# Kernel tuning notes

Measured on AMD Instinct MI355X. Metric: run time of the kernel, lower is better.

The kernel has to match this reference:

```python
import jax, jax.numpy as jnp
import numpy as np

CUTOFF = 10.0
K = 32            # max_num_neighbors
NUM_GRAPHS = 64
ATOMS = 128
N = NUM_GRAPHS * ATOMS
HID = 128
FIL = 128
NG = 50           # num_gaussians
LAYERS = 6
MAX_Z = 100
PI = 3.14159265   # constant used verbatim in the torch source


def silu(x):
    return x * jax.nn.sigmoid(x)


def build_graph(pos, batch):
    """Dense cdist + per-node top-K neighbor selection (radius_graph_pure).
    Returns idx[i,k] = k-th nearest neighbor j of center i, and a validity mask.
    Torch edge (row, col) = (j, i): node j receives a message computed from x[i].
    """
    p = jax.lax.stop_gradient(pos)
    d2 = jnp.sum((p[:, None, :] - p[None, :, :]) ** 2, -1)          # [N,N]
    same = batch[:, None] == batch[None, :]
    eye = jnp.eye(p.shape[0], dtype=bool)
    valid = same & (d2 < CUTOFF * CUTOFF) & (~eye)
    dm = jnp.where(valid, d2, jnp.inf)
    neg, idx = jax.lax.top_k(-dm, K)                                 # [N,K]
    return idx, jnp.isfinite(neg)                                    # edge valid iff within mask


def setup_inputs() -> dict:
    key = jax.random.key(0)
    ks = jax.random.split(key, 20)
    s = 0.05
    inp = {
        "pos": jax.random.normal(ks[0], (N, 3), jnp.float32),
        "z": jax.random.randint(ks[1], (N,), 0, MAX_Z),
        "batch": jnp.repeat(jnp.arange(NUM_GRAPHS), ATOMS),
        # parameters (weights stored as [in, out])
        "emb": jax.random.normal(ks[2], (MAX_Z, HID), jnp.float32) * s,
        "mw1": jax.random.normal(ks[3], (LAYERS, NG, FIL), jnp.float32) * s,
        "mb1": jax.random.normal(ks[4], (LAYERS, FIL), jnp.float32) * s,
        "mw2": jax.random.normal(ks[5], (LAYERS, FIL, FIL), jnp.float32) * s,
        "mb2": jax.random.normal(ks[6], (LAYERS, FIL), jnp.float32) * s,
        "l1w": jax.random.normal(ks[7], (LAYERS, HID, FIL), jnp.float32) * s,
        "l1b": jax.random.normal(ks[8], (LAYERS, FIL), jnp.float32) * s,
        "l2w": jax.random.normal(ks[9], (LAYERS, FIL, HID), jnp.float32) * s,
        "l2b": jax.random.normal(ks[10], (LAYERS, HID), jnp.float32) * s,
        "ow1": jax.random.normal(ks[11], (HID, HID // 2), jnp.float32) * s,
        "ob1": jax.random.normal(ks[12], (HID // 2,), jnp.float32) * s,
        "ow2": jax.random.normal(ks[13], (HID // 2, 1), jnp.float32) * s,
        "ob2": jax.random.normal(ks[14], (1,), jnp.float32) * s,
    }
    return inp


def reference(pos, z, batch, emb, mw1, mb1, mw2, mb2, l1w, l1b, l2w, l2b, ow1, ob1, ow2, ob2):
    idx, evalid = build_graph(pos, batch)                 # [N,K], [N,K]
    ev = evalid.astype(pos.dtype)
    diff = pos[idx] - pos[:, None, :]                     # [N,K,3]
    d2e = jnp.sum(diff * diff, -1)
    dist = jnp.sqrt(jnp.where(evalid, d2e, 1.0))          # safe sqrt for masked edges
    offset = jnp.linspace(0.0, CUTOFF, NG)
    width = CUTOFF / (NG - 1)
    rbf = jnp.exp(-0.5 * ((dist[..., None] - offset) / width) ** 2)   # [N,K,NG]
    cval = 0.5 * (jnp.cos(dist * PI / CUTOFF) + 1.0)
    cval = cval * (dist < CUTOFF).astype(pos.dtype) * ev  # zero out invalid edges

    h = emb[z]                                            # [N,HID]
    flat_idx = idx.reshape(-1)                            # receivers (torch row)
    for l in range(LAYERS):
        W = silu(rbf @ mw1[l] + mb1[l]) @ mw2[l] + mb2[l]           # filter MLP
        W = W * cval[..., None]                                       # [N,K,FIL]
        xj = (h @ l1w[l] + l1b[l])[:, None, :]                        # sender = center i
        msg = (xj * W).reshape(N * K, FIL)
        agg = jax.ops.segment_sum(msg, flat_idx, num_segments=N)     # scatter_add at row
        h = h + silu(agg @ l2w[l] + l2b[l])

    out = (silu(h @ ow1 + ob1) @ ow2 + ob2)[:, 0]         # [N]
    return jax.ops.segment_sum(out, batch, num_segments=NUM_GRAPHS)  # [G]
```

## Files before the change

kernel.cpp:

```cpp
#include <hip/hip_runtime.h>
#include <math.h>

typedef unsigned short u16;
typedef unsigned int   u32;
typedef unsigned long long u64;

#define NATOMS 8192
#define GRAPHS 64
#define KNN    32
#define NGAUSS 50
#define HID    128
#define LAYERS 6
#define NTAB   4096
#define SA     136
#define SW1    72
#define SH     132

typedef __attribute__((ext_vector_type(8))) short bf16x8;
typedef __attribute__((ext_vector_type(4))) float f32x4;

__device__ __forceinline__ float bf2f(u16 v) {
    return __uint_as_float(((u32)v) << 16);
}
__device__ __forceinline__ u16 f2bf(float f) {
    u32 u = __float_as_uint(f);
    u32 lsb = (u >> 16) & 1u;
    u += 0x7fffu + lsb;
    return (u16)(u >> 16);
}
__device__ __forceinline__ u32 pkbf(float lo, float hi) {
#if __has_builtin(__builtin_amdgcn_cvt_pk_bf16_f32)
    auto r = __builtin_amdgcn_cvt_pk_bf16_f32(lo, hi);
    u32 u; __builtin_memcpy(&u, &r, 4); return u;
#else
    return (u32)f2bf(lo) | ((u32)f2bf(hi) << 16);
#endif
}
__device__ __forceinline__ float silu_f(float x) {
    return x * __builtin_amdgcn_rcpf(1.0f + __expf(-x));
}
__device__ __forceinline__ bf16x8 ldfrag(const u16* p) {
    return *(const bf16x8*)__builtin_assume_aligned(p, 16);
}
__device__ __forceinline__ u64 shfl_xor_u64(u64 v, int mask) {
    u32 lo = (u32)v, hi = (u32)(v >> 32);
    lo = (u32)__shfl_xor((int)lo, mask, 64);
    hi = (u32)__shfl_xor((int)hi, mask, 64);
    return ((u64)hi << 32) | lo;
}
__device__ __forceinline__ float ldf(const void* p, int i, bool f32in) {
    return f32in ? ((const float*)p)[i] : bf2f(((const u16*)p)[i]);
}
union U8 { bf16x8 v; u32 w[4]; };

__global__ void probe_kernel(const u16* __restrict__ raw, int* __restrict__ flag,
                             int* __restrict__ rev_cnt, float* __restrict__ gsum,
                             int* __restrict__ done_cnt, int* __restrict__ xflags) {
    __shared__ int s;
    int t = threadIdx.x;
    if (t == 0) s = 0;
    __syncthreads();
    float x = bf2f(raw[2 * t]);
    if (!(fabsf(x) < 1000.0f)) atomicOr(&s, 1);
    for (int i = t; i < NATOMS; i += 256) rev_cnt[i] = 0;
    for (int i = t; i < 2048; i += 256) xflags[i] = 0;
    if (t < GRAPHS) gsum[t] = 0.0f;
    if (t == 0) *done_cnt = 0;
    __syncthreads();
    if (t == 0) *flag = s;
}

#define NARR 9
struct IngestDesc {
    const void* src[NARR];
    void*       dst[NARR];
    int         n[NARR];
};

#define NB_BUILD 2048
#define NB_PREP  768

__launch_bounds__(256)
__global__ void setup_kernel(const void* __restrict__ pos,
                             const void* __restrict__ l1w, const void* __restrict__ l2w,
                             u16* __restrict__ l1wt, u16* __restrict__ l2wt,
                             IngestDesc d, int total_ing,
                             const int* __restrict__ flag,
                             int* __restrict__ rev_cnt, u32* __restrict__ rev) {
    int bid = blockIdx.x;
    bool f32in = (*flag != 0);
    if (bid < NB_BUILD) {
        int wv = threadIdx.x >> 6, lane = threadIdx.x & 63;
        int t = bid * 4 + wv;
        int tl = t & 127;
        int base = t & ~127;
        float cx = ldf(pos, t * 3 + 0, f32in);
        float cy = ldf(pos, t * 3 + 1, f32in);
        float cz = ldf(pos, t * 3 + 2, f32in);
        u64 key[2];
#pragma unroll
        for (int c = 0; c < 2; ++c) {
            int j = lane + c * 64;
            float jx = ldf(pos, (base + j) * 3 + 0, f32in);
            float jy = ldf(pos, (base + j) * 3 + 1, f32in);
            float jz = ldf(pos, (base + j) * 3 + 2, f32in);
            float dx = __fsub_rn(cx, jx);
            float dy = __fsub_rn(cy, jy);
            float dz = __fsub_rn(cz, jz);
            float d2 = __fadd_rn(__fadd_rn(__fmul_rn(dx, dx), __fmul_rn(dy, dy)),
                                 __fmul_rn(dz, dz));
            bool valid = (j != tl) && (d2 < 100.0f);
            key[c] = valid ? ((((u64)__float_as_uint(d2)) << 32) | (u32)j) : ~0ULL;
        }
#pragma unroll
        for (int k = 2; k <= 128; k <<= 1) {
#pragma unroll
            for (int j = k >> 1; j > 0; j >>= 1) {
                if (j == 64) {
                    u64 lo = key[0] < key[1] ? key[0] : key[1];
                    u64 hi = key[0] < key[1] ? key[1] : key[0];
                    key[0] = lo; key[1] = hi;
                } else {
#pragma unroll
                    for (int r = 0; r < 2; ++r) {
                        u64 o = shfl_xor_u64(key[r], j);
                        u32 ii = (u32)(r * 64 + lane);
                        bool dir = ((ii & (u32)k) == 0);
                        bool lower = ((ii & (u32)j) == 0);
                        bool keep_min = (dir == lower);
                        bool less = key[r] < o;
                        key[r] = (less == keep_min) ? key[r] : o;
                    }
                }
            }
        }
        if (lane < KNN) {
            u64 m = key[0];
            if (m != ~0ULL) {
                float d2 = __uint_as_float((u32)(m >> 32));
                float dd = __fsqrt_rn(d2);
                if (dd < 10.0f) {
                    float u = dd * ((float)(NTAB - 1) / 10.0f);
                    int i0 = (int)(u + 0.5f);
                    if (i0 > NTAB - 1) i0 = NTAB - 1;
                    int jn = base + (int)(m & 0xffffffffu);
                    int p = atomicAdd(&rev_cnt[jn], 1);
                    rev[(size_t)jn * 128 + p] = ((u32)i0 << 7) | (u32)(t & 127);
                }
            }
        }
    } else if (bid < NB_BUILD + NB_PREP) {
        int gid = (bid - NB_BUILD) * 256 + threadIdx.x;
        int seg = gid / 98304;
        int tt = gid % 98304;
        int l = tt >> 14;
        int n = (tt >> 7) & 127;
        int k = tt & 127;
        const void* src = (seg == 0) ? l1w : l2w;
        u16* dst = (seg == 0) ? l1wt : l2wt;
        int si = l * 16384 + k * 128 + n;
        float v = f32in ? ((const float*)src)[si] : bf2f(((const u16*)src)[si]);
        dst[tt] = f2bf(v);
    } else {
        int gid = (bid - NB_BUILD - NB_PREP) * 256 + threadIdx.x;
        if (gid < total_ing) {
            int a = 0, off = gid;
            while (off >= d.n[a]) { off -= d.n[a]; ++a; }
            float v = f32in ? ((const float*)d.src[a])[off]
                            : bf2f(((const u16*)d.src[a])[off]);
            ((float*)d.dst[a])[off] = v;
        }
    }
}

__launch_bounds__(256)
__global__ void vtab_kernel(const void* __restrict__ mw1,
                            const void* __restrict__ mw2,
                            const float* __restrict__ b1,
                            const float* __restrict__ b2,
                            const int* __restrict__ flag,
                            u32* __restrict__ pk) {
    __shared__ u16 s_t1[128 * SA];
    __shared__ u16 s_w1[128 * SW1];
    __shared__ u16 s_w2[128 * SA];
    int tid = threadIdx.x;
    int l = blockIdx.x / (NTAB / 128);
    int rbase = (blockIdx.x % (NTAB / 128)) * 128;
    {
        bool f32in = (*flag != 0);
#pragma unroll
        for (int p = 0; p < 32; ++p) {
            int idx = p * 256 + tid;
            int k = idx >> 7, n = idx & 127;
            float v = (k < 50) ? ldf(mw1, l * 6400 + k * 128 + n, f32in) : 0.0f;
            s_w1[n * SW1 + k] = f2bf(v);
        }
#pragma unroll
        for (int p = 0; p < 64; ++p) {
            int idx = p * 256 + tid;
            int k = idx >> 7, n = idx & 127;
            s_w2[n * SA + k] = f2bf(ldf(mw2, l * 16384 + k * 128 + n, f32in));
        }
    }
    __syncthreads();

    int wv = tid >> 6, lane = tid & 63;
    int quad = lane >> 4, lr = lane & 15;
    int m0 = wv * 32;

    {
        const float wgi = 49.0f / 10.0f;
        const float dstep = 10.0f / (float)(NTAB - 1);
        U8 afr[2][2];
#pragma unroll
        for (int mt = 0; mt < 2; ++mt) {
            float d = (float)(rbase + m0 + mt * 16 + lr) * dstep;
            float u = d * wgi;
#pragma unroll
            for (int kki = 0; kki < 2; ++kki) {
                float t0 = u - (float)(quad * 8) - (float)(kki * 32);
                float vj[8];
#pragma unroll
                for (int j = 0; j < 8; ++j) {
                    float tt = t0 - (float)j;
                    float e = __expf(-0.5f * tt * tt);
                    if (kki == 1 && (quad * 8 + j) >= 18) e = 0.0f;
                    vj[j] = e;
                }
#pragma unroll
                for (int p = 0; p < 4; ++p)
                    afr[mt][kki].w[p] = pkbf(vj[2 * p], vj[2 * p + 1]);
            }
        }
        f32x4 accA[2][8];
#pragma unroll
        for (int mt = 0; mt < 2; ++mt)
#pragma unroll
            for (int nt = 0; nt < 8; ++nt) accA[mt][nt] = (f32x4){0.f, 0.f, 0.f, 0.f};
#pragma unroll
        for (int kki = 0; kki < 2; ++kki) {
#pragma unroll
            for (int nt = 0; nt < 8; ++nt) {
                bf16x8 b = ldfrag(&s_w1[(nt * 16 + lr) * SW1 + kki * 32 + quad * 8]);
                accA[0][nt] = __builtin_amdgcn_mfma_f32_16x16x32_bf16(afr[0][kki].v, b, accA[0][nt], 0, 0, 0);
                accA[1][nt] = __builtin_amdgcn_mfma_f32_16x16x32_bf16(afr[1][kki].v, b, accA[1][nt], 0, 0, 0);
            }
        }
#pragma unroll
        for (int mt = 0; mt < 2; ++mt) {
            int r0 = m0 + mt * 16 + quad * 4;
            u16* tp0 = &s_t1[r0 * SA + lr];
#pragma unroll
            for (int nt = 0; nt < 8; ++nt) {
                int col = nt * 16;
                float bb = b1[l * 128 + col + lr];
                u32 p01 = pkbf(silu_f(accA[mt][nt][0] + bb),
                               silu_f(accA[mt][nt][1] + bb));
                u32 p23 = pkbf(silu_f(accA[mt][nt][2] + bb),
                               silu_f(accA[mt][nt][3] + bb));
                u16* tp = tp0 + col;
                tp[0]      = (u16)p01;
                tp[SA]     = (u16)(p01 >> 16);
                tp[2 * SA] = (u16)p23;
                tp[3 * SA] = (u16)(p23 >> 16);
            }
        }
    }
    {
        f32x4 accB[2][8];
#pragma unroll
        for (int mt = 0; mt < 2; ++mt)
#pragma unroll
            for (int nt = 0; nt < 8; ++nt) accB[mt][nt] = (f32x4){0.f, 0.f, 0.f, 0.f};
#pragma unroll
        for (int kk = 0; kk < 128; kk += 32) {
            bf16x8 a0 = ldfrag(&s_t1[(m0 + lr)      * SA + kk + quad * 8]);
            bf16x8 a1 = ldfrag(&s_t1[(m0 + 16 + lr) * SA + kk + quad * 8]);
#pragma unroll
            for (int nt = 0; nt < 8; ++nt) {
                bf16x8 b = ldfrag(&s_w2[(nt * 16 + lr) * SA + kk + quad * 8]);
                accB[0][nt] = __builtin_amdgcn_mfma_f32_16x16x32_bf16(a0, b, accB[0][nt], 0, 0, 0);
                accB[1][nt] = __builtin_amdgcn_mfma_f32_16x16x32_bf16(a1, b, accB[1][nt], 0, 0, 0);
            }
        }
        const float dstep = 10.0f / (float)(NTAB - 1);
#pragma unroll
        for (int mt = 0; mt < 2; ++mt) {
            int r0 = m0 + mt * 16 + quad * 4;
            float cv[4];
#pragma unroll
            for (int r = 0; r < 4; ++r) {
                float d = (float)(rbase + r0 + r) * dstep;
                cv[r] = 0.5f * (cosf(d * 3.14159265f / 10.0f) + 1.0f);
            }
#pragma unroll
            for (int nt = 0; nt < 8; ++nt) {
                int col = nt * 16 + lr;
                float bb = b2[l * 128 + col];
#pragma unroll
                for (int r = 0; r < 4; ++r) {
                    float val = (accB[mt][nt][r] + bb) * cv[r];
                    float oth = __shfl_xor(val, 1, 64);
                    if ((lr & 1) == 0) {
                        int row = rbase + r0 + r;
                        pk[((size_t)l * NTAB + row) * 64 + (col >> 1)] =
                            pkbf(val, oth);
                    }
                }
            }
        }
    }
}

#define AGG_ISSUE(T, X, base, ev)                                              \
    {                                                                          \
        _Pragma("unroll") for (int q = 0; q < 8; ++q) {                        \
            int e = (base) + q;                                                \
            u32 pe = __builtin_amdgcn_readlane((ev), e & 63);                  \
            int sy = (int)(pe >> 7);                                           \
            int sx = (int)(pe & 127u);                                         \
            T[q] = pkl[(size_t)sy * 64 + lane];                                \
            X[q] = *(const u32*)&s_x[sx * SA + c2];                            \
        }                                                                      \
    }

#define AGG_COMPUTE(T, X)                                                      \
    {                                                                          \
        _Pragma("unroll") for (int q = 0; q < 8; ++q) {                        \
            float v0 = bf2f((u16)T[q]) * bf2f((u16)X[q]);                      \
            float v1 = bf2f((u16)(T[q] >> 16)) * bf2f((u16)(X[q] >> 16));      \
            switch (q & 3) {                                                   \
                case 0: a0 += v0; a1 += v1; break;                             \
                case 1: b0 += v0; b1v += v1; break;                            \
                case 2: c0 += v0; c1 += v1; break;                             \
                default: d0 += v0; d1 += v1; break;                            \
            }                                                                  \
        }                                                                      \
    }

__launch_bounds__(1024, 1)
__global__ void graph_kernel(const int* __restrict__ rev_cnt,
                             const u32* __restrict__ rev,
                             const u32* __restrict__ pk,
                             const int* __restrict__ z,
                             const float* __restrict__ emb,
                             const u16* __restrict__ l1wt,
                             const float* __restrict__ l1b,
                             const u16* __restrict__ l2wt,
                             const float* __restrict__ l2b,
                             const float* __restrict__ ow1,
                             const float* __restrict__ ob1,
                             const float* __restrict__ ow2,
                             const float* __restrict__ ob2,
                             u32* __restrict__ xbuf,
                             int* __restrict__ xflags,
                             float* __restrict__ gsum,
                             int* __restrict__ done_cnt,
                             void* __restrict__ out,
                             const int* __restrict__ flag) {
    __shared__ __align__(16) u16 s_x[128 * SA];
    __shared__ __align__(16) u16 s_hb[64 * SA];
    __shared__ __align__(16) u16 s_pair[2 * 64 * SA];
    __shared__ float s_b1a[LAYERS * 128];
    __shared__ float s_b2a[LAYERS * 128];
    __shared__ int s_perm[32];
    __shared__ float s_sum;
    __shared__ int s_last;

    u16* s_ahi = s_pair;
    u16* s_alo = s_pair + 64 * SA;

    int tid = threadIdx.x;
    int bid = blockIdx.x;
    int g = bid & 63, q4 = bid >> 6;
    int abase = g * 128;
    int rbase = q4 * 32;
    int w = tid >> 6, lane = tid & 63;
    int quad = lane >> 4, lr = lane & 15;
    int rowt = (w >> 3) * 16;
    int coln = (w & 7) * 16;
    int c2 = lane * 2;

    float hreg[4];

    for (int i = tid; i < LAYERS * 128; i += 1024) {
        s_b1a[i] = l1b[i];
        s_b2a[i] = l2b[i];
    }

    if (w == 0) {
        u32 key = 0;
        if (lane < 32) {
            int dg = rev_cnt[abase + rbase + lane];
            key = ((u32)dg << 8) | (u32)lane;
        }
#pragma unroll
        for (int k = 2; k <= 64; k <<= 1) {
#pragma unroll
            for (int j = k >> 1; j > 0; j >>= 1) {
                u32 o = (u32)__shfl_xor((int)key, j, 64);
                bool dir = ((lane & k) == 0);
                bool lower = ((lane & j) == 0);
                bool keep_max = (dir == lower);
                bool greater = key > o;
                key = (greater == keep_max) ? key : o;
            }
        }
        if (lane < 32) s_perm[lane] = (int)(key & 0xffu);
    }

    {
        int r = tid >> 5, cb = (tid & 31) * 4;
        const float* src = emb + (size_t)z[abase + rbase + r] * 128 + cb;
        float4 v = *(const float4*)src;
        u32* dd = (u32*)&s_hb[r * SA + cb];
        dd[0] = pkbf(v.x, v.y); dd[1] = pkbf(v.z, v.w);
    }
    __syncthreads();

    int rloc[2];
    rloc[0] = s_perm[w];
    rloc[1] = s_perm[31 - w];
    int dgv[2];
    u32 eAv[2], eBv[2];
#pragma unroll
    for (int rr = 0; rr < 2; ++rr) {
        int j = abase + rbase + rloc[rr];
        dgv[rr] = rev_cnt[j];
        eAv[rr] = rev[(size_t)j * 128 + lane];
        eBv[rr] = (dgv[rr] > 64) ? rev[(size_t)j * 128 + 64 + lane] : eAv[rr];
    }

    {
        f32x4 acc = (f32x4){0.f, 0.f, 0.f, 0.f};
#pragma unroll
        for (int kk = 0; kk < 128; kk += 32) {
            bf16x8 a = ldfrag(&s_hb[(rowt + lr) * SA + kk + quad * 8]);
            bf16x8 b = ldfrag(l1wt + (coln + lr) * 128 + kk + quad * 8);
            acc = __builtin_amdgcn_mfma_f32_16x16x32_bf16(a, b, acc, 0, 0, 0);
        }
#pragma unroll
        for (int r = 0; r < 4; ++r) {
            int col = coln + lr;
            s_x[(rbase + rowt + quad * 4 + r) * SA + col] =
                f2bf(acc[r] + s_b1a[col]);
        }
    }

    for (int l = 0; l <= LAYERS; ++l) {
        if (l < LAYERS) {
            int e = l;
            u64* xbw = (u64*)(xbuf + ((size_t)bid * 2 + (e & 1)) * 2048);
            __syncthreads();
            {
                u64 v = *(const u64*)&s_x[(rbase + (tid >> 5)) * SA +
                                          (tid & 31) * 4];
                __hip_atomic_store(&xbw[tid], v, __ATOMIC_RELAXED,
                                   __HIP_MEMORY_SCOPE_SYSTEM);
            }
            __syncthreads();
            if (tid == 0)
                __hip_atomic_store(&xflags[(g * 4 + q4) * 8 + e], 1,
                                   __ATOMIC_RELAXED, __HIP_MEMORY_SCOPE_SYSTEM);
            if (tid < 3) {
                int pq = (q4 + 1 + tid) & 3;
                const int* pf = &xflags[(g * 4 + pq) * 8 + e];
                while (__hip_atomic_load(pf, __ATOMIC_RELAXED,
                                         __HIP_MEMORY_SCOPE_SYSTEM) == 0)
                    __builtin_amdgcn_s_sleep(1);
            }
            __syncthreads();
#pragma unroll
            for (int k = 0; k < 3; ++k) {
                int pq = (q4 + 1 + k) & 3;
                const u64* xbr = (const u64*)(xbuf +
                    ((size_t)(g + 64 * pq) * 2 + (e & 1)) * 2048);
                u64 v = __hip_atomic_load(&xbr[tid], __ATOMIC_RELAXED,
                                          __HIP_MEMORY_SCOPE_SYSTEM);
                *(u64*)&s_x[(pq * 32 + (tid >> 5)) * SA + (tid & 31) * 4] = v;
            }
            __syncthreads();
        }
        if (l == LAYERS) break;

        const u32* pkl = pk + (size_t)l * NTAB * 64;

#pragma unroll
        for (int rr = 0; rr < 2; ++rr) {
            int row = rloc[rr];
            int deg = dgv[rr];
            u32 e0 = eAv[rr];
            u32 e1 = eBv[rr];
            float a0 = 0.f, a1 = 0.f, b0 = 0.f, b1v = 0.f;
            float c0 = 0.f, c1 = 0.f, d0 = 0.f, d1 = 0.f;
            u32 tA[8], xA[8], tB[8], xB[8];
            int ng = deg >> 3;
            if (ng > 0) {
                AGG_ISSUE(tA, xA, 0, e0);
                int gi = 1;
                for (; gi + 1 < ng; gi += 2) {
                    u32 evB = (gi < 8) ? e0 : e1;
                    AGG_ISSUE(tB, xB, gi * 8, evB);
                    AGG_COMPUTE(tA, xA);
                    u32 evA = ((gi + 1) < 8) ? e0 : e1;
                    AGG_ISSUE(tA, xA, (gi + 1) * 8, evA);
                    AGG_COMPUTE(tB, xB);
                }
                if (gi < ng) {
                    u32 evB = (gi < 8) ? e0 : e1;
                    AGG_ISSUE(tB, xB, gi * 8, evB);
                    AGG_COMPUTE(tA, xA);
                    AGG_COMPUTE(tB, xB);
                } else {
                    AGG_COMPUTE(tA, xA);
                }
            }
            for (int it = ng * 8; it < deg; ++it) {
                u32 ev = (it < 64) ? e0 : e1;
                u32 pe = __builtin_amdgcn_readlane(ev, it & 63);
                int sy = (int)(pe >> 7);
                int sx = (int)(pe & 127u);
                u32 t = pkl[(size_t)sy * 64 + lane];
                u32 x = *(const u32*)&s_x[sx * SA + c2];
                a0 += bf2f((u16)t) * bf2f((u16)x);
                a1 += bf2f((u16)(t >> 16)) * bf2f((u16)(x >> 16));
            }
            float sxv = (a0 + b0) + (c0 + d0);
            float syv = (a1 + b1v) + (c1 + d1);
            u32 hp = pkbf(sxv, syv);
            u32 lp = pkbf(sxv - bf2f((u16)hp), syv - bf2f((u16)(hp >> 16)));
            *(u32*)&s_ahi[row * SA + c2] = hp;
            *(u32*)&s_alo[row * SA + c2] = lp;
        }
        __syncthreads();

        {
            const u16* B2t = l2wt + (size_t)l * 16384;
            f32x4 acc = (f32x4){0.f, 0.f, 0.f, 0.f};
#pragma unroll
            for (int kk = 0; kk < 128; kk += 32) {
                bf16x8 ah = ldfrag(&s_ahi[(rowt + lr) * SA + kk + quad * 8]);
                bf16x8 al = ldfrag(&s_alo[(rowt + lr) * SA + kk + quad * 8]);
                bf16x8 b = ldfrag(B2t + (coln + lr) * 128 + kk + quad * 8);
                acc = __builtin_amdgcn_mfma_f32_16x16x32_bf16(ah, b, acc, 0, 0, 0);
                acc = __builtin_amdgcn_mfma_f32_16x16x32_bf16(al, b, acc, 0, 0, 0);
            }
            if (l == LAYERS - 1 && tid == 0) s_sum = 0.0f;
            int col = coln + lr;
#pragma unroll
            for (int r = 0; r < 4; ++r) {
                int row = rowt + quad * 4 + r;
                float hold = (l == 0)
                    ? emb[(size_t)z[abase + rbase + row] * 128 + col]
                    : hreg[r];
                float hn = hold + silu_f(acc[r] + s_b2a[l * 128 + col]);
                hreg[r] = hn;
                if (l < LAYERS - 1) s_hb[row * SA + col] = f2bf(hn);
            }
        }
        __syncthreads();

        if (l < LAYERS - 1) {
            const u16* B1n = l1wt + (size_t)(l + 1) * 16384;
            f32x4 ac2 = (f32x4){0.f, 0.f, 0.f, 0.f};
#pragma unroll
            for (int kk = 0; kk < 128; kk += 32) {
                bf16x8 a = ldfrag(&s_hb[(rowt + lr) * SA + kk + quad * 8]);
                bf16x8 b = ldfrag(B1n + (coln + lr) * 128 + kk + quad * 8);
                ac2 = __builtin_amdgcn_mfma_f32_16x16x32_bf16(a, b, ac2, 0, 0, 0);
            }
            int col = coln + lr;
#pragma unroll
            for (int r = 0; r < 4; ++r) {
                s_x[(rbase + rowt + quad * 4 + r) * SA + col] =
                    f2bf(ac2[r] + s_b1a[(l + 1) * 128 + col]);
            }
        } else {
            float* s_hf = (float*)s_pair;
            float* s_w  = (float*)s_x;
            {
                float4* dst = (float4*)s_w;
                const float4* src4 = (const float4*)ow1;
                dst[tid] = src4[tid];
                dst[tid + 1024] = src4[tid + 1024];
            }
#pragma unroll
            for (int r = 0; r < 4; ++r)
                s_hf[(rowt + quad * 4 + r) * SH + coln + lr] = hreg[r];
            __syncthreads();
            int atom = tid >> 5, cg = tid & 31;
            const float* hr = &s_hf[atom * SH];
            float ax = 0.f, ay = 0.f;
#pragma unroll 8
            for (int f = 0; f < 128; ++f) {
                float hv = hr[f];
                float2 wv = ((const float2*)&s_w[f * 64])[cg];
                ax += hv * wv.x; ay += hv * wv.y;
            }
            int c0i = cg * 2;
            float v = silu_f(ax + ob1[c0i + 0]) * ow2[c0i + 0]
                    + silu_f(ay + ob1[c0i + 1]) * ow2[c0i + 1];
            v += __shfl_xor(v, 1, 64);
            v += __shfl_xor(v, 2, 64);
            v += __shfl_xor(v, 4, 64);
            v += __shfl_xor(v, 8, 64);
            v += __shfl_xor(v, 16, 64);
            if ((tid & 31) == 0) atomicAdd(&s_sum, v + ob2[0]);
            __syncthreads();
            if (tid == 0) {
                atomicAdd(&gsum[g], s_sum);
                __threadfence();
                int tk = __hip_atomic_fetch_add(done_cnt, 1, __ATOMIC_ACQ_REL,
                                                __HIP_MEMORY_SCOPE_AGENT);
                s_last = (tk == 4 * GRAPHS - 1);
            }
            __syncthreads();
            if (s_last && tid < GRAPHS) {
                float gg = __hip_atomic_load(&gsum[tid], __ATOMIC_RELAXED,
                                             __HIP_MEMORY_SCOPE_AGENT);
                if (*flag) ((float*)out)[tid] = gg;
                else       ((u16*)out)[tid]   = f2bf(gg);
            }
            break;
        }
    }
}

extern "C" void kernel_launch(void* const* d_in, const int* in_sizes, int n_in,
                              void* d_out, int out_size, void* d_ws, size_t ws_size,
                              hipStream_t stream) {
    const void* pos  = d_in[0];
    const int*  z    = (const int*)d_in[1];
    const void* emb  = d_in[3];
    const void* mw1  = d_in[4];
    const void* mb1  = d_in[5];
    const void* mw2  = d_in[6];
    const void* mb2  = d_in[7];
    const void* l1w  = d_in[8];
    const void* l1b  = d_in[9];
    const void* l2w  = d_in[10];
    const void* l2b  = d_in[11];
    const void* ow1  = d_in[12];
    const void* ob1  = d_in[13];
    const void* ow2  = d_in[14];
    const void* ob2  = d_in[15];

    char* ws = (char*)d_ws;
    const size_t KB = 1024, MB = 1048576;
    int*   w_flag  = (int*)  (ws);
    int*   w_done  = (int*)  (ws + 64);
    int*   w_xfl   = (int*)  (ws + 8 * KB);
    float* c_emb   = (float*)(ws + 112 * KB);
    float* c_mb1   = (float*)(ws + 168 * KB);
    float* c_mb2   = (float*)(ws + 176 * KB);
    float* c_l1b   = (float*)(ws + 184 * KB);
    float* c_l2b   = (float*)(ws + 192 * KB);
    float* c_ow1   = (float*)(ws + 200 * KB);
    float* c_ob1   = (float*)(ws + 236 * KB);
    float* c_ow2   = (float*)(ws + 240 * KB);
    float* c_ob2   = (float*)(ws + 244 * KB);
    float* w_gsum  = (float*)(ws + 248 * KB);
    u16*   c_l1wt  = (u16*)  (ws + 256 * KB);
    u16*   c_l2wt  = (u16*)  (ws + 448 * KB);
    int*   rev_cnt = (int*)  (ws + 2  * MB);
    u32*   w_rev   = (u32*)  (ws + 3  * MB);
    u32*   w_pk    = (u32*)  (ws + 21 * MB);
    u32*   w_xbuf  = (u32*)  (ws + 28 * MB);

    probe_kernel<<<1, 256, 0, stream>>>((const u16*)emb, w_flag, rev_cnt,
                                        w_gsum, w_done, w_xfl);

    IngestDesc dsc;
    const void* srcs[NARR] = {emb, mb1, mb2, l1b, l2b, ow1, ob1, ow2, ob2};
    void* dsts[NARR] = {c_emb, c_mb1, c_mb2, c_l1b, c_l2b, c_ow1, c_ob1,
                        c_ow2, c_ob2};
    int ns_[NARR] = {12800, 768, 768, 768, 768, 8192, 64, 64, 1};
    int total = 0;
    for (int a = 0; a < NARR; ++a) {
        dsc.src[a] = srcs[a]; dsc.dst[a] = dsts[a]; dsc.n[a] = ns_[a];
        total += ns_[a];
    }
    int nb_ing = (total + 255) / 256;
    setup_kernel<<<NB_BUILD + NB_PREP + nb_ing, 256, 0, stream>>>(
        pos, l1w, l2w, c_l1wt, c_l2wt, dsc, total, w_flag, rev_cnt, w_rev);

    vtab_kernel<<<LAYERS * NTAB / 128, 256, 0, stream>>>(
        mw1, mw2, c_mb1, c_mb2, w_flag, w_pk);

    graph_kernel<<<4 * GRAPHS, 1024, 0, stream>>>(
        rev_cnt, w_rev, w_pk, z, c_emb, c_l1wt, c_l1b, c_l2wt, c_l2b,
        c_ow1, c_ob1, c_ow2, c_ob2, w_xbuf, w_xfl,
        w_gsum, w_done, d_out, w_flag);
}
```

Before: 233.6 us.

## Balance receiver rows across the four blocks of each graph by degree

The kernel now sorts all 128 atoms of a graph by reverse-edge degree with a 128-element bitonic sort, replacing the per-32-row sort. It deals the sorted rows to the four blocks in a snake pattern, so each block gets a similar total degree instead of a fixed contiguous quarter. The aim is to even out aggregation work across the blocks that synchronise every layer through flags, cutting time spent waiting on the slowest block. In exchange, every s_x and embedding access becomes indirect through a shared permutation table, and the sort in one wave is larger.

Result: faster. 228.4 us (median of 2 runs) (-2.2%).

```diff
diff --git a/kernel.cpp b/kernel.cpp
--- a/kernel.cpp
+++ b/kernel.cpp
@@ -363,7 +363,7 @@
     __shared__ __align__(16) u16 s_pair[2 * 64 * SA];
     __shared__ float s_b1a[LAYERS * 128];
     __shared__ float s_b2a[LAYERS * 128];
-    __shared__ int s_perm[32];
+    __shared__ int s_gp[4][32];
     __shared__ float s_sum;
     __shared__ int s_last;
 
@@ -374,7 +374,6 @@
     int bid = blockIdx.x;
     int g = bid & 63, q4 = bid >> 6;
     int abase = g * 128;
-    int rbase = q4 * 32;
     int w = tid >> 6, lane = tid & 63;
     int quad = lane >> 4, lr = lane & 15;
     int rowt = (w >> 3) * 16;
@@ -389,47 +388,69 @@
     }
 
     if (w == 0) {
-        u32 key = 0;
-        if (lane < 32) {
-            int dg = rev_cnt[abase + rbase + lane];
-            key = ((u32)dg << 8) | (u32)lane;
-        }
-#pragma unroll
-        for (int k = 2; k <= 64; k <<= 1) {
+        u32 key[2];
+#pragma unroll
+        for (int c = 0; c < 2; ++c) {
+            int rowi = lane + c * 64;
+            int dg = rev_cnt[abase + rowi];
+            key[c] = ((u32)dg << 8) | (u32)rowi;
+        }
+#pragma unroll
+        for (int k = 2; k <= 128; k <<= 1) {
 #pragma unroll
             for (int j = k >> 1; j > 0; j >>= 1) {
-                u32 o = (u32)__shfl_xor((int)key, j, 64);
-                bool dir = ((lane & k) == 0);
-                bool lower = ((lane & j) == 0);
-                bool keep_max = (dir == lower);
-                bool greater = key > o;
-                key = (greater == keep_max) ? key : o;
-            }
-        }
-        if (lane < 32) s_perm[lane] = (int)(key & 0xffu);
-    }
+                if (j == 64) {
+                    u32 mx = key[0] > key[1] ? key[0] : key[1];
+                    u32 mn = key[0] > key[1] ? key[1] : key[0];
+                    key[0] = mx; key[1] = mn;
+                } else {
+#pragma unroll
+                    for (int r = 0; r < 2; ++r) {
+                        u32 o = (u32)__shfl_xor((int)key[r], j, 64);
+                        u32 ii = (u32)(r * 64 + lane);
+                        bool dir = ((ii & (u32)k) == 0);
+                        bool lower = ((ii & (u32)j) == 0);
+                        bool keep_max = (dir == lower);
+                        bool greater = key[r] > o;
+                        key[r] = (greater == keep_max) ? key[r] : o;
+                    }
+                }
+            }
+        }
+#pragma unroll
+        for (int c = 0; c < 2; ++c) {
+            int p = lane + c * 64;
+            int r = p >> 2, cc = p & 3;
+            int q = (r & 1) ? (3 - cc) : cc;
+            s_gp[q][r] = (int)(key[c] & 0xffu);
+        }
+    }
+    __syncthreads();
 
     {
         int r = tid >> 5, cb = (tid & 31) * 4;
-        const float* src = emb + (size_t)z[abase + rbase + r] * 128 + cb;
+        const float* src = emb + (size_t)z[abase + s_gp[q4][r]] * 128 + cb;
         float4 v = *(const float4*)src;
         u32* dd = (u32*)&s_hb[r * SA + cb];
         dd[0] = pkbf(v.x, v.y); dd[1] = pkbf(v.z, v.w);
     }
-    __syncthreads();
 
     int rloc[2];
-    rloc[0] = s_perm[w];
-    rloc[1] = s_perm[31 - w];
+    rloc[0] = w;
+    rloc[1] = 31 - w;
+    int grow[2];
+    grow[0] = s_gp[q4][rloc[0]];
+    grow[1] = s_gp[q4][rloc[1]];
     int dgv[2];
     u32 eAv[2], eBv[2];
 #pragma unroll
     for (int rr = 0; rr < 2; ++rr) {
-        int j = abase + rbase + rloc[rr];
+        int j = abase + grow[rr];
         dgv[rr] = rev_cnt[j];
         eAv[rr] = rev[(size_t)j * 128 + lane];
         eBv[rr] = (dgv[rr] > 64) ? rev[(size_t)j * 128 + 64 + lane] : eAv[rr];
     }
+    __syncthreads();
 
     {
         f32x4 acc = (f32x4){0.f, 0.f, 0.f, 0.f};
@@ -442,7 +463,7 @@
 #pragma unroll
         for (int r = 0; r < 4; ++r) {
             int col = coln + lr;
-            s_x[(rbase + rowt + quad * 4 + r) * SA + col] =
+            s_x[s_gp[q4][rowt + quad * 4 + r] * SA + col] =
                 f2bf(acc[r] + s_b1a[col]);
         }
     }
@@ -453,7 +474,7 @@
             u64* xbw = (u64*)(xbuf + ((size_t)bid * 2 + (e & 1)) * 2048);
             __syncthreads();
             {
-                u64 v = *(const u64*)&s_x[(rbase + (tid >> 5)) * SA +
+                u64 v = *(const u64*)&s_x[s_gp[q4][tid >> 5] * SA +
                                           (tid & 31) * 4];
                 __hip_atomic_store(&xbw[tid], v, __ATOMIC_RELAXED,
                                    __HIP_MEMORY_SCOPE_SYSTEM);
@@ -477,7 +498,7 @@
                     ((size_t)(g + 64 * pq) * 2 + (e & 1)) * 2048);
                 u64 v = __hip_atomic_load(&xbr[tid], __ATOMIC_RELAXED,
                                           __HIP_MEMORY_SCOPE_SYSTEM);
-                *(u64*)&s_x[(pq * 32 + (tid >> 5)) * SA + (tid & 31) * 4] = v;
+                *(u64*)&s_x[s_gp[pq][tid >> 5] * SA + (tid & 31) * 4] = v;
             }
             __syncthreads();
         }
@@ -551,7 +572,7 @@
             for (int r = 0; r < 4; ++r) {
                 int row = rowt + quad * 4 + r;
                 float hold = (l == 0)
-                    ? emb[(size_t)z[abase + rbase + row] * 128 + col]
+                    ? emb[(size_t)z[abase + s_gp[q4][row]] * 128 + col]
                     : hreg[r];
                 float hn = hold + silu_f(acc[r] + s_b2a[l * 128 + col]);
                 hreg[r] = hn;
@@ -572,7 +593,7 @@
             int col = coln + lr;
 #pragma unroll
             for (int r = 0; r < 4; ++r) {
-                s_x[(rbase + rowt + quad * 4 + r) * SA + col] =
+                s_x[s_gp[q4][rowt + quad * 4 + r] * SA + col] =
                     f2bf(ac2[r] + s_b1a[(l + 1) * 128 + col]);
             }
         } else {
```
